# Kernel optimization log

Hardware: AMD Instinct MI355X
Metric: run time of the kernel (lower is better)

Reference implementation:

```python
import jax, jax.numpy as jnp
import numpy as np
import math

B, T, N, D = 8, 4, 2048, 256
M, E = 4096, 8

def setup_inputs() -> dict:
    key = jax.random.key(0)
    ks = jax.random.split(key, 8)
    std = 0.02
    return {
        "prop_embed": jax.random.normal(ks[0], (B, T, N, D), jnp.float32),
        "adap_embed": jax.random.normal(ks[1], (B, N, D), jnp.float32),
        "x_proj_w": jax.random.normal(ks[2], (D, D), jnp.float32) * (1.0 / np.sqrt(D)),
        "x_proj_b": jnp.zeros((D,), jnp.float32),
        "keyMatrix": jax.random.normal(ks[3], (M, D), jnp.float32) * std,
        "memMatrix": jax.random.normal(ks[4], (M, D), jnp.float32) * std,
        "w_gate": jax.random.normal(ks[5], (D, E), jnp.float32) * (1.0 / np.sqrt(D)),
        "w_noise": jax.random.normal(ks[6], (D, E), jnp.float32) * (1.0 / np.sqrt(D)),
    }

def reference(prop_embed, adap_embed, x_proj_w, x_proj_b, keyMatrix, memMatrix, w_gate, w_noise):
    b, t, n, d = prop_embed.shape
    m = memMatrix.shape[0]
    x = jnp.mean(prop_embed, axis=1)                      # [B,N,D]
    q = jnp.tanh(x @ x_proj_w.T + x_proj_b)               # [B,N,D]
    att = jnp.einsum('bnd,md->bnm', q, keyMatrix)         # [B,N,M]
    # eval mode: noise_stddev * self.training == 0, so noisy_logits == clean_logits
    clean_logits = memMatrix @ w_gate                     # [M,E]
    mem_label = jax.nn.softmax(clean_logits, axis=-1)     # [M,E]
    # sparse_qk: keep top-k = int(ln(M)) logits, rest -> -inf
    k = int(math.log(m))
    vals, idx = jax.lax.top_k(att, k)                     # [B,N,k]
    att2 = jnp.full((b * n, m), -jnp.inf, dtype=att.dtype)
    rows = jnp.arange(b * n)[:, None]
    att2 = att2.at[rows, idx.reshape(b * n, k)].set(vals.reshape(b * n, k))
    att_w = jax.nn.softmax(att2, axis=-1).reshape(b, n, m)
    mem_retrieved = jnp.einsum('bnm,md->bnd', att_w, memMatrix)
    label_retrieved = jnp.einsum('bnm,me->bne', att_w, mem_label)
    gate = label_retrieved
    return (gate, mem_retrieved, label_retrieved, mem_label, att_w)
```

## Files before the change

kernel.cpp:

```cpp
#include <hip/hip_runtime.h>
#include <hip/hip_fp16.h>
#include <math.h>

#define Bb 8
#define Tt 4
#define Nn 2048
#define Dd 256
#define Mm 4096
#define Ee 8
#define ROWS (Bb*Nn)
#define KSEL 8
#define KC 16

#define O_GATE 0LL
#define O_MEMR 131072LL
#define O_LABR 4325376LL
#define O_MLAB 4456448LL
#define O_ATTW 4489216LL

#define WS_WT    0LL
#define WS_KH    262144LL
#define WS_ATTH  16777216LL
#define WS_QH    150994944LL

typedef float f32x4 __attribute__((ext_vector_type(4)));
typedef short short8 __attribute__((ext_vector_type(8)));
typedef _Float16 f16x8 __attribute__((ext_vector_type(8)));

__device__ __forceinline__ unsigned short f2h(float x) {
    __half h = __float2half(x);
    return *reinterpret_cast<unsigned short*>(&h);
}

__device__ __forceinline__ void gload_lds16(const void* g, void* l) {
    __builtin_amdgcn_global_load_lds(
        (const __attribute__((address_space(1))) unsigned int*)g,
        (__attribute__((address_space(3))) unsigned int*)l,
        16, 0, 0);
}

__global__ void k_transpose(const float* __restrict__ W, float* __restrict__ WT) {
    int i = blockIdx.x * 256 + threadIdx.x;
    int r = i >> 8, c = i & 255;
    WT[c * 256 + r] = W[r * 256 + c];
}

__global__ __launch_bounds__(256) void k_q(const float* __restrict__ prop,
                                           const float* __restrict__ WT,
                                           const float* __restrict__ bias,
                                           float* __restrict__ qf,
                                           unsigned short* __restrict__ qh) {
    __shared__ float xs[16][256];
    int tid = threadIdx.x;
    int row0 = blockIdx.x * 16;
    #pragma unroll
    for (int r = 0; r < 16; ++r) {
        int row = row0 + r;
        int b = row >> 11;
        int n = row & 2047;
        const float* p = prop + ((long long)(b * Tt) * Nn + n) * Dd + tid;
        float s = 0.f;
        #pragma unroll
        for (int t = 0; t < Tt; ++t) s += p[(long long)t * Nn * Dd];
        xs[r][tid] = s * 0.25f;
    }
    __syncthreads();
    float acc[16];
    #pragma unroll
    for (int r = 0; r < 16; ++r) acc[r] = 0.f;
    int c = tid;
    for (int d = 0; d < 256; ++d) {
        float wv = WT[d * 256 + c];
        #pragma unroll
        for (int r = 0; r < 16; ++r) acc[r] = fmaf(xs[r][d], wv, acc[r]);
    }
    float bv = bias[c];
    #pragma unroll
    for (int r = 0; r < 16; ++r) {
        float qv = tanhf(acc[r] + bv);
        long long o = (long long)(row0 + r) * Dd + c;
        qf[o] = qv;
        qh[o] = f2h(qv);
    }
}

__global__ void k_key16(const float* __restrict__ key, unsigned short* __restrict__ kh) {
    int idx = blockIdx.x * 256 + threadIdx.x;
    kh[idx] = f2h(key[idx]);
}

__global__ __launch_bounds__(256) void k_mlabel(const float* __restrict__ mem,
                                                const float* __restrict__ wg,
                                                float* __restrict__ mlab) {
    int m = blockIdx.x * 256 + threadIdx.x;
    if (m >= Mm) return;
    float acc[Ee];
    #pragma unroll
    for (int e = 0; e < Ee; ++e) acc[e] = 0.f;
    const float* mr = mem + (long long)m * Dd;
    for (int d = 0; d < Dd; ++d) {
        float mv = mr[d];
        #pragma unroll
        for (int e = 0; e < Ee; ++e) acc[e] = fmaf(mv, wg[d * Ee + e], acc[e]);
    }
    float mx = acc[0];
    #pragma unroll
    for (int e = 1; e < Ee; ++e) mx = fmaxf(mx, acc[e]);
    float z = 0.f;
    #pragma unroll
    for (int e = 0; e < Ee; ++e) { acc[e] = expf(acc[e] - mx); z += acc[e]; }
    float inv = 1.f / z;
    #pragma unroll
    for (int e = 0; e < Ee; ++e) mlab[(long long)m * Ee + e] = acc[e] * inv;
}

__global__ __launch_bounds__(256) void k_att(const unsigned short* __restrict__ qh,
                                             const unsigned short* __restrict__ kh,
                                             unsigned short* __restrict__ attH) {
    __shared__ __align__(16) unsigned short smem[8192];
    int bid = blockIdx.x;
    int swz = (bid & 7) * 512 + (bid >> 3);
    int bx = swz & 31;
    int by = swz >> 5;
    int tid = threadIdx.x;
    int lane = tid & 63, w = tid >> 6;
    int wr = w >> 1, wc = w & 1;
    long long row0 = (long long)by * 128;
    long long col0 = (long long)bx * 128;

    f32x4 acc[4][4];
    #pragma unroll
    for (int m = 0; m < 4; ++m)
        #pragma unroll
        for (int n = 0; n < 4; ++n) acc[m][n] = (f32x4){0.f, 0.f, 0.f, 0.f};

    int rr = lane >> 2;
    int sp = lane & 3;

    auto stage = [&](int k0) {
        #pragma unroll
        for (int t = 0; t < 2; ++t) {
            const unsigned short* src = t ? kh : qh;
            long long b0 = t ? col0 : row0;
            #pragma unroll
            for (int i = 0; i < 2; ++i) {
                int r = w * 32 + i * 16 + rr;
                int sl = sp ^ ((r >> 1) & 3);
                const unsigned short* g = src + (b0 + r) * 256 + k0 * 32 + sl * 8;
                unsigned short* l = smem + t * 4096 + (w * 32 + i * 16) * 32;
                gload_lds16(g, l);
            }
        }
    };

    stage(0);
    for (int k0 = 0; k0 < 8; ++k0) {
        __syncthreads();
        int lr = lane & 15, j = lane >> 4;
        f16x8 ah[4], bh[4];
        #pragma unroll
        for (int m = 0; m < 4; ++m) {
            int r = wr * 64 + m * 16 + lr;
            int off = r * 32 + ((j ^ ((r >> 1) & 3)) * 8);
            ah[m] = *(const f16x8*)(smem + off);
        }
        #pragma unroll
        for (int n = 0; n < 4; ++n) {
            int r = wc * 64 + n * 16 + lr;
            int off = r * 32 + ((j ^ ((r >> 1) & 3)) * 8);
            bh[n] = *(const f16x8*)(smem + 4096 + off);
        }
        #pragma unroll
        for (int m = 0; m < 4; ++m)
            #pragma unroll
            for (int n = 0; n < 4; ++n)
                acc[m][n] = __builtin_amdgcn_mfma_f32_16x16x32_f16(ah[m], bh[n], acc[m][n], 0, 0, 0);
        if (k0 < 7) { __syncthreads(); stage(k0 + 1); }
    }

    int lr = lane & 15, j = lane >> 4;
    #pragma unroll
    for (int m = 0; m < 4; ++m)
        #pragma unroll
        for (int n = 0; n < 4; ++n) {
            long long C = col0 + wc * 64 + n * 16 + lr;
            #pragma unroll
            for (int reg = 0; reg < 4; ++reg) {
                long long R = row0 + wr * 64 + m * 16 + j * 4 + reg;
                attH[R * Mm + C] = f2h(acc[m][n][reg]);
            }
        }
}

__global__ __launch_bounds__(256) void k_final2(const unsigned short* __restrict__ attH,
                                                const float* __restrict__ qf,
                                                const float* __restrict__ key,
                                                const float* __restrict__ mem,
                                                const float* __restrict__ mlab,
                                                float* __restrict__ gate,
                                                float* __restrict__ memr,
                                                float* __restrict__ labr,
                                                float* __restrict__ attw) {
    int tid = threadIdx.x;
    int lane = tid & 63;
    long long row = (long long)blockIdx.x * 4 + (tid >> 6);
    const unsigned short* arow = attH + row * Mm;

    unsigned int v[8];
    #pragma unroll
    for (int s = 0; s < 8; ++s) v[s] = 0u;

    #pragma unroll
    for (int t = 0; t < 8; ++t) {
        int c8 = t * 64 + lane;
        short8 x8 = *(const short8*)(arow + c8 * 8);
        unsigned int rb = (unsigned)(4095 - c8 * 8);
        #pragma unroll
        for (int jj = 0; jj < 8; ++jj) {
            unsigned int b = (unsigned short)x8[jj];
            unsigned int sr = (unsigned)((int)(b << 16) >> 31);
            unsigned int mono = b ^ ((sr >> 17) | 0x8000u);
            unsigned int keyv = (mono << 16) | (rb - jj);
            if (keyv > v[7]) {
                unsigned int x = keyv;
                #pragma unroll
                for (int s = 0; s < 8; ++s) {
                    unsigned int hi = v[s] > x ? v[s] : x;
                    unsigned int lo = v[s] > x ? x : v[s];
                    v[s] = hi; x = lo;
                }
            }
        }
    }

    unsigned int sk[KC];
    #pragma unroll
    for (int k = 0; k < KC; ++k) {
        unsigned int bv = v[0];
        #pragma unroll
        for (int d = 1; d < 64; d <<= 1) {
            unsigned int ov = (unsigned)__shfl_xor((int)bv, d);
            bv = bv > ov ? bv : ov;
        }
        sk[k] = bv;
        bool won = (v[0] == bv);
        #pragma unroll
        for (int s = 0; s < 7; ++s) v[s] = won ? v[s + 1] : v[s];
        v[7] = won ? 0u : v[7];
    }

    int civ[KC];
    #pragma unroll
    for (int s = 0; s < KC; ++s) civ[s] = 4095 - (int)(sk[s] & 0xFFFFu);

    int c = lane & 15, g = lane >> 4;
    int cidx = civ[0];
    #pragma unroll
    for (int s = 1; s < KC; ++s) cidx = (c == s) ? civ[s] : cidx;
    const float* qrow = qf + row * Dd;
    const float* krow = key + (long long)cidx * Dd;
    double dacc = 0.0;
    #pragma unroll
    for (int i = 0; i < 16; ++i) {
        float4 qv = *(const float4*)(qrow + g * 64 + i * 4);
        float4 kv = *(const float4*)(krow + g * 64 + i * 4);
        dacc = fma((double)qv.x, (double)kv.x, dacc);
        dacc = fma((double)qv.y, (double)kv.y, dacc);
        dacc = fma((double)qv.z, (double)kv.z, dacc);
        dacc = fma((double)qv.w, (double)kv.w, dacc);
    }
    dacc += __shfl_xor(dacc, 16);
    dacc += __shfl_xor(dacc, 32);
    float rvf = (float)dacc;

    float cv[KC];
    #pragma unroll
    for (int s = 0; s < KC; ++s) cv[s] = __shfl(rvf, s);

    unsigned int m32[KC];
    #pragma unroll
    for (int s = 0; s < KC; ++s) {
        unsigned int fb = __float_as_uint(cv[s]);
        m32[s] = fb ^ ((unsigned)((int)fb >> 31) | 0x80000000u);
    }
    bool sel[KC];
    #pragma unroll
    for (int s = 0; s < KC; ++s) {
        int r = 0;
        #pragma unroll
        for (int t = 0; t < KC; ++t) {
            if (t != s) {
                bool gt = (m32[t] > m32[s]) || (m32[t] == m32[s] && civ[t] < civ[s]);
                r += gt ? 1 : 0;
            }
        }
        sel[s] = (r < KSEL);
    }

    float mx = cv[0];
    #pragma unroll
    for (int s = 1; s < KC; ++s) mx = fmaxf(mx, cv[s]);
    float p[KC]; float z = 0.f;
    #pragma unroll
    for (int s = 0; s < KC; ++s) { p[s] = sel[s] ? expf(cv[s] - mx) : 0.f; z += p[s]; }
    float inv = 1.f / z;
    #pragma unroll
    for (int s = 0; s < KC; ++s) p[s] *= inv;

    {
        float4 a = make_float4(0.f, 0.f, 0.f, 0.f);
        #pragma unroll
        for (int s = 0; s < KC; ++s) {
            if (sel[s]) {
                const float4 mv = *(const float4*)(mem + (long long)civ[s] * Dd + lane * 4);
                a.x = fmaf(p[s], mv.x, a.x); a.y = fmaf(p[s], mv.y, a.y);
                a.z = fmaf(p[s], mv.z, a.z); a.w = fmaf(p[s], mv.w, a.w);
            }
        }
        *(float4*)(memr + row * Dd + lane * 4) = a;
    }

    if (lane < Ee) {
        float s8 = 0.f;
        #pragma unroll
        for (int s = 0; s < KC; ++s)
            if (sel[s]) s8 = fmaf(p[s], mlab[(long long)civ[s] * Ee + lane], s8);
        gate[row * Ee + lane] = s8;
        labr[row * Ee + lane] = s8;
    }

    float* awrow = attw + row * Mm;
    {
        f32x4 zz = (f32x4){0.f, 0.f, 0.f, 0.f};
        #pragma unroll
        for (int t = 0; t < 16; ++t)
            __builtin_nontemporal_store(zz, (f32x4*)(awrow + (t * 64 + lane) * 4));
    }
    __syncthreads();
    if (lane < KC) {
        float myp = p[0]; int myi = civ[0];
        #pragma unroll
        for (int s = 1; s < KC; ++s) {
            myp = (lane == s) ? p[s] : myp;
            myi = (lane == s) ? civ[s] : myi;
        }
        awrow[myi] = myp;
    }
}

extern "C" void kernel_launch(void* const* d_in, const int* in_sizes, int n_in,
                              void* d_out, int out_size, void* d_ws, size_t ws_size,
                              hipStream_t stream) {
    const float* prop = (const float*)d_in[0];
    const float* W    = (const float*)d_in[2];
    const float* bias = (const float*)d_in[3];
    const float* key  = (const float*)d_in[4];
    const float* mem  = (const float*)d_in[5];
    const float* wg   = (const float*)d_in[6];

    float* out  = (float*)d_out;
    float* gate = out + O_GATE;
    float* memr = out + O_MEMR;
    float* labr = out + O_LABR;
    float* mlab = out + O_MLAB;
    float* attw = out + O_ATTW;

    char* ws = (char*)d_ws;
    float*          WT   = (float*)(ws + WS_WT);
    unsigned short* kh   = (unsigned short*)(ws + WS_KH);
    unsigned short* attH = (unsigned short*)(ws + WS_ATTH);
    unsigned short* qh   = (unsigned short*)(ws + WS_QH);
    float*          qf   = memr;

    k_transpose<<<256, 256, 0, stream>>>(W, WT);
    k_q<<<ROWS / 16, 256, 0, stream>>>(prop, WT, bias, qf, qh);
    k_key16<<<(Mm * Dd) / 256, 256, 0, stream>>>(key, kh);
    k_mlabel<<<Mm / 256, 256, 0, stream>>>(mem, wg, mlab);
    k_att<<<4096, 256, 0, stream>>>(qh, kh, attH);
    k_final2<<<ROWS / 4, 256, 0, stream>>>(attH, qf, key, mem, mlab, gate, memr, labr, attw);
}
```

Measured before the change: 276.3 us.

## Fuse fp16 attention GEMM with streaming top-k selection, drop score matrix

Replaces the separate fp16 score GEMM (which wrote a full 16384x4096 half matrix to workspace) and the top-k kernel with one kernel. Each wave computes 16x16 MFMA tiles for its 16 rows across all keys and keeps a per-lane running top-8 list with a threshold, then merges across lanes and rescores candidates in double precision. This removes the large intermediate write and read-back, at the cost of lower MFMA reuse: each wave streams all of K from global or L2 with no LDS sharing, plus heavy per-tile VALU insertion work. The attw scatter is deferred to after the zeroing stores, going through LDS and a block barrier.

```diff
diff --git a/kernel.cpp b/kernel.cpp
--- a/kernel.cpp
+++ b/kernel.cpp
@@ -20,23 +20,14 @@
 
 #define WS_WT    0LL
 #define WS_KH    262144LL
-#define WS_ATTH  16777216LL
-#define WS_QH    150994944LL
+#define WS_QH    2359296LL
 
 typedef float f32x4 __attribute__((ext_vector_type(4)));
-typedef short short8 __attribute__((ext_vector_type(8)));
 typedef _Float16 f16x8 __attribute__((ext_vector_type(8)));
 
 __device__ __forceinline__ unsigned short f2h(float x) {
     __half h = __float2half(x);
     return *reinterpret_cast<unsigned short*>(&h);
-}
-
-__device__ __forceinline__ void gload_lds16(const void* g, void* l) {
-    __builtin_amdgcn_global_load_lds(
-        (const __attribute__((address_space(1))) unsigned int*)g,
-        (__attribute__((address_space(3))) unsigned int*)l,
-        16, 0, 0);
 }
 
 __global__ void k_transpose(const float* __restrict__ W, float* __restrict__ WT) {
@@ -114,237 +105,212 @@
     for (int e = 0; e < Ee; ++e) mlab[(long long)m * Ee + e] = acc[e] * inv;
 }
 
-__global__ __launch_bounds__(256) void k_att(const unsigned short* __restrict__ qh,
-                                             const unsigned short* __restrict__ kh,
-                                             unsigned short* __restrict__ attH) {
-    __shared__ __align__(16) unsigned short smem[8192];
-    int bid = blockIdx.x;
-    int swz = (bid & 7) * 512 + (bid >> 3);
-    int bx = swz & 31;
-    int by = swz >> 5;
+__global__ __launch_bounds__(256) void k_rank(const unsigned short* __restrict__ qh,
+                                              const unsigned short* __restrict__ kh,
+                                              const float* __restrict__ qf,
+                                              const float* __restrict__ key,
+                                              const float* __restrict__ mem,
+                                              const float* __restrict__ mlab,
+                                              float* __restrict__ gate,
+                                              float* __restrict__ memr,
+                                              float* __restrict__ labr,
+                                              float* __restrict__ attw) {
+    __shared__ float lds_p[4][16][16];
+    __shared__ int   lds_i[4][16][16];
     int tid = threadIdx.x;
     int lane = tid & 63, w = tid >> 6;
-    int wr = w >> 1, wc = w & 1;
-    long long row0 = (long long)by * 128;
-    long long col0 = (long long)bx * 128;
-
-    f32x4 acc[4][4];
-    #pragma unroll
-    for (int m = 0; m < 4; ++m)
-        #pragma unroll
-        for (int n = 0; n < 4; ++n) acc[m][n] = (f32x4){0.f, 0.f, 0.f, 0.f};
-
-    int rr = lane >> 2;
-    int sp = lane & 3;
-
-    auto stage = [&](int k0) {
-        #pragma unroll
-        for (int t = 0; t < 2; ++t) {
-            const unsigned short* src = t ? kh : qh;
-            long long b0 = t ? col0 : row0;
-            #pragma unroll
-            for (int i = 0; i < 2; ++i) {
-                int r = w * 32 + i * 16 + rr;
-                int sl = sp ^ ((r >> 1) & 3);
-                const unsigned short* g = src + (b0 + r) * 256 + k0 * 32 + sl * 8;
-                unsigned short* l = smem + t * 4096 + (w * 32 + i * 16) * 32;
-                gload_lds16(g, l);
+    int lr = lane & 15, j = lane >> 4;
+    long long row0 = (long long)blockIdx.x * 64 + w * 16;
+
+    f16x8 af[8];
+    #pragma unroll
+    for (int k0 = 0; k0 < 8; ++k0)
+        af[k0] = *(const f16x8*)(qh + (row0 + lr) * 256 + k0 * 32 + j * 8);
+
+    unsigned int L[4][8];
+    float thr[4];
+    #pragma unroll
+    for (int r = 0; r < 4; ++r) {
+        thr[r] = -INFINITY;
+        #pragma unroll
+        for (int s = 0; s < 8; ++s) L[r][s] = 0u;
+    }
+
+    f16x8 bbA[8], bbB[8];
+    #pragma unroll
+    for (int k0 = 0; k0 < 8; ++k0)
+        bbA[k0] = *(const f16x8*)(kh + (long long)lr * 256 + k0 * 32 + j * 8);
+
+    auto process = [&](const f16x8* bb, int t) {
+        f32x4 acc = (f32x4){0.f, 0.f, 0.f, 0.f};
+        #pragma unroll
+        for (int k0 = 0; k0 < 8; ++k0)
+            acc = __builtin_amdgcn_mfma_f32_16x16x32_f16(af[k0], bb[k0], acc, 0, 0, 0);
+        unsigned int colkey = (unsigned)(4095 - (t * 16 + lr));
+        #pragma unroll
+        for (int r = 0; r < 4; ++r) {
+            float x = acc[r];
+            if (x > thr[r]) {
+                unsigned int fb = __float_as_uint(x);
+                unsigned int mono = fb ^ ((unsigned)((int)fb >> 31) | 0x80000000u);
+                unsigned int xx = (mono & 0xFFFFF000u) | colkey;
+                #pragma unroll
+                for (int s = 0; s < 8; ++s) {
+                    unsigned int hi = L[r][s] > xx ? L[r][s] : xx;
+                    unsigned int lo = L[r][s] > xx ? xx : L[r][s];
+                    L[r][s] = hi; xx = lo;
+                }
+                unsigned int h20 = L[r][7] & 0xFFFFF000u;
+                float nt = (h20 >= 0x80000000u) ? __uint_as_float(h20 ^ 0x80000000u)
+                                                : __uint_as_float(~h20);
+                thr[r] = (h20 == 0u) ? -INFINITY : nt;
             }
         }
     };
 
-    stage(0);
-    for (int k0 = 0; k0 < 8; ++k0) {
-        __syncthreads();
-        int lr = lane & 15, j = lane >> 4;
-        f16x8 ah[4], bh[4];
-        #pragma unroll
-        for (int m = 0; m < 4; ++m) {
-            int r = wr * 64 + m * 16 + lr;
-            int off = r * 32 + ((j ^ ((r >> 1) & 3)) * 8);
-            ah[m] = *(const f16x8*)(smem + off);
+    for (int t2 = 0; t2 < 256; t2 += 2) {
+        #pragma unroll
+        for (int k0 = 0; k0 < 8; ++k0)
+            bbB[k0] = *(const f16x8*)(kh + (long long)((t2 + 1) * 16 + lr) * 256 + k0 * 32 + j * 8);
+        process(bbA, t2);
+        if (t2 + 2 < 256) {
+            #pragma unroll
+            for (int k0 = 0; k0 < 8; ++k0)
+                bbA[k0] = *(const f16x8*)(kh + (long long)((t2 + 2) * 16 + lr) * 256 + k0 * 32 + j * 8);
         }
-        #pragma unroll
-        for (int n = 0; n < 4; ++n) {
-            int r = wc * 64 + n * 16 + lr;
-            int off = r * 32 + ((j ^ ((r >> 1) & 3)) * 8);
-            bh[n] = *(const f16x8*)(smem + 4096 + off);
+        process(bbB, t2 + 1);
+        if ((t2 & 15) == 14) __builtin_amdgcn_s_barrier();
+    }
+
+    #pragma unroll
+    for (int r = 0; r < 4; ++r) {
+        unsigned int ck[KC];
+        #pragma unroll
+        for (int k = 0; k < KC; ++k) {
+            unsigned int bv = L[r][0];
+            #pragma unroll
+            for (int d = 1; d < 16; d <<= 1) {
+                unsigned int ov = (unsigned)__shfl_xor((int)bv, d);
+                bv = bv > ov ? bv : ov;
+            }
+            ck[k] = bv;
+            bool won = (L[r][0] == bv);
+            #pragma unroll
+            for (int s = 0; s < 7; ++s) L[r][s] = won ? L[r][s + 1] : L[r][s];
+            L[r][7] = won ? 0u : L[r][7];
         }
-        #pragma unroll
-        for (int m = 0; m < 4; ++m)
-            #pragma unroll
-            for (int n = 0; n < 4; ++n)
-                acc[m][n] = __builtin_amdgcn_mfma_f32_16x16x32_f16(ah[m], bh[n], acc[m][n], 0, 0, 0);
-        if (k0 < 7) { __syncthreads(); stage(k0 + 1); }
-    }
-
-    int lr = lane & 15, j = lane >> 4;
-    #pragma unroll
-    for (int m = 0; m < 4; ++m)
-        #pragma unroll
-        for (int n = 0; n < 4; ++n) {
-            long long C = col0 + wc * 64 + n * 16 + lr;
-            #pragma unroll
-            for (int reg = 0; reg < 4; ++reg) {
-                long long R = row0 + wr * 64 + m * 16 + j * 4 + reg;
-                attH[R * Mm + C] = f2h(acc[m][n][reg]);
-            }
+
+        for (int jj = 0; jj < 4; ++jj) {
+            long long row = row0 + jj * 4 + r;
+            int rloc = jj * 4 + r;
+
+            int civ[KC];
+            #pragma unroll
+            for (int s = 0; s < KC; ++s) {
+                unsigned int cks = (unsigned)__shfl((int)ck[s], jj * 16);
+                civ[s] = 4095 - (int)(cks & 0xFFFu);
+            }
+
+            int cidx = civ[0];
+            #pragma unroll
+            for (int s = 1; s < KC; ++s) cidx = (lr == s) ? civ[s] : cidx;
+            const float* qrow = qf + row * Dd;
+            const float* krow = key + (long long)cidx * Dd;
+            double d0 = 0.0, d1 = 0.0, d2 = 0.0, d3 = 0.0;
+            #pragma unroll
+            for (int i = 0; i < 16; ++i) {
+                float4 qv = *(const float4*)(qrow + j * 64 + i * 4);
+                float4 kv = *(const float4*)(krow + j * 64 + i * 4);
+                d0 = fma((double)qv.x, (double)kv.x, d0);
+                d1 = fma((double)qv.y, (double)kv.y, d1);
+                d2 = fma((double)qv.z, (double)kv.z, d2);
+                d3 = fma((double)qv.w, (double)kv.w, d3);
+            }
+            double dacc = (d0 + d1) + (d2 + d3);
+            dacc += __shfl_xor(dacc, 16);
+            dacc += __shfl_xor(dacc, 32);
+            float rvf = (float)dacc;
+            float cv[KC];
+            #pragma unroll
+            for (int s = 0; s < KC; ++s) cv[s] = __shfl(rvf, s);
+
+            unsigned int m32[KC];
+            #pragma unroll
+            for (int s = 0; s < KC; ++s) {
+                unsigned int fb = __float_as_uint(cv[s]);
+                m32[s] = fb ^ ((unsigned)((int)fb >> 31) | 0x80000000u);
+            }
+            bool sel[KC];
+            #pragma unroll
+            for (int s = 0; s < KC; ++s) {
+                int rk = 0;
+                #pragma unroll
+                for (int t = 0; t < KC; ++t) {
+                    if (t != s) {
+                        bool gt = (m32[t] > m32[s]) || (m32[t] == m32[s] && civ[t] < civ[s]);
+                        rk += gt ? 1 : 0;
+                    }
+                }
+                sel[s] = (rk < KSEL);
+            }
+
+            float mx = cv[0];
+            #pragma unroll
+            for (int s = 1; s < KC; ++s) mx = fmaxf(mx, cv[s]);
+            float p[KC]; float z = 0.f;
+            #pragma unroll
+            for (int s = 0; s < KC; ++s) { p[s] = sel[s] ? expf(cv[s] - mx) : 0.f; z += p[s]; }
+            float inv = 1.f / z;
+            #pragma unroll
+            for (int s = 0; s < KC; ++s) p[s] *= inv;
+
+            {
+                float4 a = make_float4(0.f, 0.f, 0.f, 0.f);
+                #pragma unroll
+                for (int s = 0; s < KC; ++s) {
+                    if (sel[s]) {
+                        const float4 mv = *(const float4*)(mem + (long long)civ[s] * Dd + lane * 4);
+                        a.x = fmaf(p[s], mv.x, a.x); a.y = fmaf(p[s], mv.y, a.y);
+                        a.z = fmaf(p[s], mv.z, a.z); a.w = fmaf(p[s], mv.w, a.w);
+                    }
+                }
+                *(float4*)(memr + row * Dd + lane * 4) = a;
+            }
+            if (lane < Ee) {
+                float s8 = 0.f;
+                #pragma unroll
+                for (int s = 0; s < KC; ++s)
+                    if (sel[s]) s8 = fmaf(p[s], mlab[(long long)civ[s] * Ee + lane], s8);
+                gate[row * Ee + lane] = s8;
+                labr[row * Ee + lane] = s8;
+            }
+            if (lane < KC) {
+                float myp = p[0]; int myi = civ[0];
+                #pragma unroll
+                for (int s = 1; s < KC; ++s) {
+                    myp = (lane == s) ? p[s] : myp;
+                    myi = (lane == s) ? civ[s] : myi;
+                }
+                lds_p[w][rloc][lane] = myp;
+                lds_i[w][rloc][lane] = myi;
+            }
+            float* awrow = attw + row * Mm;
+            f32x4 zz = (f32x4){0.f, 0.f, 0.f, 0.f};
+            #pragma unroll
+            for (int tt = 0; tt < 16; ++tt)
+                __builtin_nontemporal_store(zz, (f32x4*)(awrow + (tt * 64 + lane) * 4));
         }
-}
-
-__global__ __launch_bounds__(256) void k_final2(const unsigned short* __restrict__ attH,
-                                                const float* __restrict__ qf,
-                                                const float* __restrict__ key,
-                                                const float* __restrict__ mem,
-                                                const float* __restrict__ mlab,
-                                                float* __restrict__ gate,
-                                                float* __restrict__ memr,
-                                                float* __restrict__ labr,
-                                                float* __restrict__ attw) {
-    int tid = threadIdx.x;
-    int lane = tid & 63;
-    long long row = (long long)blockIdx.x * 4 + (tid >> 6);
-    const unsigned short* arow = attH + row * Mm;
-
-    unsigned int v[8];
-    #pragma unroll
-    for (int s = 0; s < 8; ++s) v[s] = 0u;
-
-    #pragma unroll
-    for (int t = 0; t < 8; ++t) {
-        int c8 = t * 64 + lane;
-        short8 x8 = *(const short8*)(arow + c8 * 8);
-        unsigned int rb = (unsigned)(4095 - c8 * 8);
-        #pragma unroll
-        for (int jj = 0; jj < 8; ++jj) {
-            unsigned int b = (unsigned short)x8[jj];
-            unsigned int sr = (unsigned)((int)(b << 16) >> 31);
-            unsigned int mono = b ^ ((sr >> 17) | 0x8000u);
-            unsigned int keyv = (mono << 16) | (rb - jj);
-            if (keyv > v[7]) {
-                unsigned int x = keyv;
-                #pragma unroll
-                for (int s = 0; s < 8; ++s) {
-                    unsigned int hi = v[s] > x ? v[s] : x;
-                    unsigned int lo = v[s] > x ? x : v[s];
-                    v[s] = hi; x = lo;
-                }
-            }
-        }
-    }
-
-    unsigned int sk[KC];
-    #pragma unroll
-    for (int k = 0; k < KC; ++k) {
-        unsigned int bv = v[0];
-        #pragma unroll
-        for (int d = 1; d < 64; d <<= 1) {
-            unsigned int ov = (unsigned)__shfl_xor((int)bv, d);
-            bv = bv > ov ? bv : ov;
-        }
-        sk[k] = bv;
-        bool won = (v[0] == bv);
-        #pragma unroll
-        for (int s = 0; s < 7; ++s) v[s] = won ? v[s + 1] : v[s];
-        v[7] = won ? 0u : v[7];
-    }
-
-    int civ[KC];
-    #pragma unroll
-    for (int s = 0; s < KC; ++s) civ[s] = 4095 - (int)(sk[s] & 0xFFFFu);
-
-    int c = lane & 15, g = lane >> 4;
-    int cidx = civ[0];
-    #pragma unroll
-    for (int s = 1; s < KC; ++s) cidx = (c == s) ? civ[s] : cidx;
-    const float* qrow = qf + row * Dd;
-    const float* krow = key + (long long)cidx * Dd;
-    double dacc = 0.0;
-    #pragma unroll
-    for (int i = 0; i < 16; ++i) {
-        float4 qv = *(const float4*)(qrow + g * 64 + i * 4);
-        float4 kv = *(const float4*)(krow + g * 64 + i * 4);
-        dacc = fma((double)qv.x, (double)kv.x, dacc);
-        dacc = fma((double)qv.y, (double)kv.y, dacc);
-        dacc = fma((double)qv.z, (double)kv.z, dacc);
-        dacc = fma((double)qv.w, (double)kv.w, dacc);
-    }
-    dacc += __shfl_xor(dacc, 16);
-    dacc += __shfl_xor(dacc, 32);
-    float rvf = (float)dacc;
-
-    float cv[KC];
-    #pragma unroll
-    for (int s = 0; s < KC; ++s) cv[s] = __shfl(rvf, s);
-
-    unsigned int m32[KC];
-    #pragma unroll
-    for (int s = 0; s < KC; ++s) {
-        unsigned int fb = __float_as_uint(cv[s]);
-        m32[s] = fb ^ ((unsigned)((int)fb >> 31) | 0x80000000u);
-    }
-    bool sel[KC];
-    #pragma unroll
-    for (int s = 0; s < KC; ++s) {
-        int r = 0;
-        #pragma unroll
-        for (int t = 0; t < KC; ++t) {
-            if (t != s) {
-                bool gt = (m32[t] > m32[s]) || (m32[t] == m32[s] && civ[t] < civ[s]);
-                r += gt ? 1 : 0;
-            }
-        }
-        sel[s] = (r < KSEL);
-    }
-
-    float mx = cv[0];
-    #pragma unroll
-    for (int s = 1; s < KC; ++s) mx = fmaxf(mx, cv[s]);
-    float p[KC]; float z = 0.f;
-    #pragma unroll
-    for (int s = 0; s < KC; ++s) { p[s] = sel[s] ? expf(cv[s] - mx) : 0.f; z += p[s]; }
-    float inv = 1.f / z;
-    #pragma unroll
-    for (int s = 0; s < KC; ++s) p[s] *= inv;
-
-    {
-        float4 a = make_float4(0.f, 0.f, 0.f, 0.f);
-        #pragma unroll
-        for (int s = 0; s < KC; ++s) {
-            if (sel[s]) {
-                const float4 mv = *(const float4*)(mem + (long long)civ[s] * Dd + lane * 4);
-                a.x = fmaf(p[s], mv.x, a.x); a.y = fmaf(p[s], mv.y, a.y);
-                a.z = fmaf(p[s], mv.z, a.z); a.w = fmaf(p[s], mv.w, a.w);
-            }
-        }
-        *(float4*)(memr + row * Dd + lane * 4) = a;
-    }
-
-    if (lane < Ee) {
-        float s8 = 0.f;
-        #pragma unroll
-        for (int s = 0; s < KC; ++s)
-            if (sel[s]) s8 = fmaf(p[s], mlab[(long long)civ[s] * Ee + lane], s8);
-        gate[row * Ee + lane] = s8;
-        labr[row * Ee + lane] = s8;
-    }
-
-    float* awrow = attw + row * Mm;
-    {
-        f32x4 zz = (f32x4){0.f, 0.f, 0.f, 0.f};
-        #pragma unroll
-        for (int t = 0; t < 16; ++t)
-            __builtin_nontemporal_store(zz, (f32x4*)(awrow + (t * 64 + lane) * 4));
-    }
+    }
+
     __syncthreads();
-    if (lane < KC) {
-        float myp = p[0]; int myi = civ[0];
-        #pragma unroll
-        for (int s = 1; s < KC; ++s) {
-            myp = (lane == s) ? p[s] : myp;
-            myi = (lane == s) ? civ[s] : myi;
-        }
-        awrow[myi] = myp;
+
+    #pragma unroll
+    for (int i = 0; i < 4; ++i) {
+        int e = lane * 4 + i;
+        int rl = e >> 4, sl = e & 15;
+        float pv = lds_p[w][rl][sl];
+        int iv = lds_i[w][rl][sl];
+        attw[(row0 + rl) * Mm + iv] = pv;
     }
 }
 
@@ -366,16 +332,14 @@
     float* attw = out + O_ATTW;
 
     char* ws = (char*)d_ws;
-    float*          WT   = (float*)(ws + WS_WT);
-    unsigned short* kh   = (unsigned short*)(ws + WS_KH);
-    unsigned short* attH = (unsigned short*)(ws + WS_ATTH);
-    unsigned short* qh   = (unsigned short*)(ws + WS_QH);
-    float*          qf   = memr;
+    float*          WT = (float*)(ws + WS_WT);
+    unsigned short* kh = (unsigned short*)(ws + WS_KH);
+    unsigned short* qh = (unsigned short*)(ws + WS_QH);
+    float*          qf = memr;
 
     k_transpose<<<256, 256, 0, stream>>>(W, WT);
     k_q<<<ROWS / 16, 256, 0, stream>>>(prop, WT, bias, qf, qh);
     k_key16<<<(Mm * Dd) / 256, 256, 0, stream>>>(key, kh);
     k_mlabel<<<Mm / 256, 256, 0, stream>>>(mem, wg, mlab);
-    k_att<<<4096, 256, 0, stream>>>(qh, kh, attH);
-    k_final2<<<ROWS / 4, 256, 0, stream>>>(attH, qf, key, mem, mlab, gate, memr, labr, attw);
-}
+    k_rank<<<ROWS / 64, 256, 0, stream>>>(qh, kh, qf, key, mem, mlab, gate, memr, labr, attw);
+}
```

After: 573.6 us. 108% more time.
